# Performance work log

Hardware: AMD Instinct MI355X
Metric: run time of the kernel (lower is better)

## Reference

```python
import jax, jax.numpy as jnp
import numpy as np

N = 100001          # 1000 DAGs * (99 tasks + 1 summary) + 1 global node
E = 3200000
IN_DIM = 8
H = 64
N_DAGS = 1000
TEMPERATURE = 1.0


def setup_inputs() -> dict:
    key = jax.random.key(0)
    ks = jax.random.split(key, 12)
    x = jax.random.normal(ks[0], (N, IN_DIM), dtype=jnp.float32)
    flags = jax.random.bernoulli(ks[1], 0.5, (N,)).astype(jnp.float32)
    x = x.at[:, -1].set(flags)  # last feature column is the schedule flag
    edge_index = jax.random.randint(ks[2], (2, E), 0, N, dtype=jnp.int32)
    dag_summary_index = jnp.arange(N_DAGS, dtype=jnp.int32) * 100 + 99

    def w(k, shape, fan_in):
        return jax.random.normal(k, shape, dtype=jnp.float32) / np.float32(np.sqrt(fan_in))

    return {
        'x': x,
        'edge_index': edge_index,
        'dag_summary_index': dag_summary_index,
        'W1': w(ks[3], (IN_DIM, H), IN_DIM), 'b1': jnp.zeros((H,), jnp.float32),
        'W2': w(ks[4], (H, H), H),           'b2': jnp.zeros((H,), jnp.float32),
        'M1': w(ks[5], (3 * H, H), 3 * H),   'mb1': jnp.zeros((H,), jnp.float32),
        'M2': w(ks[6], (H, H), H),           'mb2': jnp.zeros((H,), jnp.float32),
        'M3': w(ks[7], (H, 1), H),           'mb3': jnp.zeros((1,), jnp.float32),
    }


def _gcn_conv(x, src, dst, W, b):
    # PyG GCNConv: add self-loops, symmetric normalization, linear, scatter-add, bias
    n = x.shape[0]
    loop = jnp.arange(n, dtype=src.dtype)
    s = jnp.concatenate([src, loop])
    d = jnp.concatenate([dst, loop])
    deg = jax.ops.segment_sum(jnp.ones_like(s, dtype=x.dtype), d, num_segments=n)
    dinv = jnp.where(deg > 0, jax.lax.rsqrt(deg), 0.0)
    norm = dinv[s] * dinv[d]                      # [E+N]
    h = x @ W                                     # [N, H]
    msg = h[s] * norm[:, None]                    # gather + scale (memory-bound)
    return jax.ops.segment_sum(msg, d, num_segments=n) + b


def reference(x, edge_index, dag_summary_index, W1, b1, W2, b2, M1, mb1, M2, mb2, M3, mb3):
    src, dst = edge_index[0], edge_index[1]
    h = jax.nn.relu(_gcn_conv(x, src, dst, W1, b1))
    h = jax.nn.relu(_gcn_conv(h, src, dst, W2, b2))   # [N, H]

    n = x.shape[0]
    idx = jnp.arange(n - 1)
    # dag_idx for node i == number of summary indices <= i (matches loop increment)
    dag_of = jnp.searchsorted(dag_summary_index, idx, side='right')
    dag_of = jnp.clip(dag_of, 0, dag_summary_index.shape[0] - 1)
    dag_emb = h[dag_summary_index[dag_of]]            # [N-1, H]
    global_emb = jnp.broadcast_to(h[-1], (n - 1, h.shape[1]))
    combined = jnp.concatenate([h[:-1], dag_emb, global_emb], axis=1)  # [N-1, 3H]

    z = jax.nn.relu(combined @ M1 + mb1)
    z = jax.nn.relu(z @ M2 + mb2)
    scores = (z @ M3 + mb3)[:, 0]                     # [N-1]

    flags = x[:-1, -1]
    is_summary = jnp.zeros((n,), bool).at[dag_summary_index].set(True)[:-1]
    mask = (flags == 1.0) & (~is_summary)
    probs = jax.nn.softmax(jnp.where(mask, scores / TEMPERATURE, -jnp.inf))
    selected = jnp.argmax(probs)                      # is_sampling=False path
    return probs, selected
```

## Files before the change

### kernel.cpp

```cpp
#include <hip/hip_runtime.h>
#include <math.h>

#define CHUNK 8192


__global__ void __launch_bounds__(256) k_bcount(const int* __restrict__ dst, int e,
                                                int* __restrict__ bcount) {
    __shared__ int c[256];
    int t = threadIdx.x;
    c[t] = 0;
    __syncthreads();
    for (int i = blockIdx.x * 256 + t; i < e; i += gridDim.x * 256)
        atomicAdd(&c[dst[i] >> 9], 1);
    __syncthreads();
    if (c[t]) atomicAdd(&bcount[t], c[t]);
}

__global__ void k_bscan(const int* __restrict__ bcount, int nb, int e,
                        int* __restrict__ bbase, int* __restrict__ bcur) {
    __shared__ int s[256];
    int t = threadIdx.x;
    int v = (t < nb) ? bcount[t] : 0;
    s[t] = v;
    __syncthreads();
    for (int d = 1; d < 256; d <<= 1) {
        int a = (t >= d) ? s[t - d] : 0;
        __syncthreads();
        s[t] += a;
        __syncthreads();
    }
    if (t < nb) { bbase[t] = s[t] - v; bcur[t] = s[t] - v; }
    if (t == 0) bbase[nb] = e;
}

__global__ void __launch_bounds__(256) k_bscatter(const int* __restrict__ src,
                                                  const int* __restrict__ dst, int e,
                                                  int* __restrict__ bcur,
                                                  int2* __restrict__ pairs) {
    __shared__ unsigned short rank[CHUNK];
    __shared__ int cnt[256];
    __shared__ int base[256];
    int t = threadIdx.x;
    int c0 = blockIdx.x * CHUNK;
    cnt[t] = 0;
    __syncthreads();
#pragma unroll
    for (int k = 0; k < CHUNK / 256; k++) {
        int i = c0 + k * 256 + t;
        if (i < e) {
            int b = dst[i] >> 9;
            rank[k * 256 + t] = (unsigned short)atomicAdd(&cnt[b], 1);
        }
    }
    __syncthreads();
    int cb = cnt[t];
    base[t] = cb ? atomicAdd(&bcur[t], cb) : 0;
    __syncthreads();
#pragma unroll
    for (int k = 0; k < CHUNK / 256; k++) {
        int i = c0 + k * 256 + t;
        if (i < e) {
            int d = dst[i];
            int b = d >> 9;
            pairs[base[b] + rank[k * 256 + t]] = make_int2(src[i], d);
        }
    }
}

__global__ void __launch_bounds__(256) k_bdeg(const int2* __restrict__ pairs,
                                              const int* __restrict__ bbase,
                                              int* __restrict__ deg, int* __restrict__ off,
                                              float* __restrict__ dinv, int n) {
    __shared__ int h[512];
    int t = threadIdx.x, b = blockIdx.x;
    h[t] = 0; h[t + 256] = 0;
    __syncthreads();
    int s0 = bbase[b], s1 = bbase[b + 1];
    int nbase = b << 9;
    for (int i = s0 + t; i < s1; i += 256)
        atomicAdd(&h[pairs[i].y - nbase], 1);
    __syncthreads();
    int o0 = h[t], o1 = h[t + 256];
    for (int d = 1; d < 512; d <<= 1) {
        int a0 = (t >= d) ? h[t - d] : 0;
        int a1 = (t + 256 >= d) ? h[t + 256 - d] : 0;
        __syncthreads();
        h[t] += a0; h[t + 256] += a1;
        __syncthreads();
    }
    int n0 = nbase + t, n1 = nbase + t + 256;
    if (n0 < n) { deg[n0] = o0; off[n0] = s0 + h[t] - o0; dinv[n0] = rsqrtf((float)(o0 + 1)); }
    if (n1 < n) { deg[n1] = o1; off[n1] = s0 + h[t + 256] - o1; dinv[n1] = rsqrtf((float)(o1 + 1)); }
}

__global__ void __launch_bounds__(256) k_bcsr(const int2* __restrict__ pairs,
                                              const int* __restrict__ bbase,
                                              const int* __restrict__ off,
                                              int* __restrict__ csr, int n) {
    __shared__ int curL[512];
    __shared__ int offL[512];
    int t = threadIdx.x, b = blockIdx.x;
    int nbase = b << 9;
    curL[t] = 0; curL[t + 256] = 0;
    int n0 = nbase + t, n1 = nbase + t + 256;
    offL[t] = (n0 < n) ? off[n0] : 0;
    offL[t + 256] = (n1 < n) ? off[n1] : 0;
    __syncthreads();
    int s0 = bbase[b], s1 = bbase[b + 1];
    for (int i = s0 + t; i < s1; i += 256) {
        int2 p = pairs[i];
        int local = p.y - nbase;
        int r = atomicAdd(&curL[local], 1);
        csr[offL[local] + r] = p.x;
    }
}


__global__ void k_xs(const float* __restrict__ x, const float* __restrict__ dinv,
                     float* __restrict__ xs, int n) {
    int t = blockIdx.x * blockDim.x + threadIdx.x;
    if (t >= n * 8) return;
    xs[t] = x[t] * dinv[t >> 3];
}


__global__ void __launch_bounds__(256) k_conv8(const float* __restrict__ xs,
                                               const int* __restrict__ csr,
                                               const int* __restrict__ off,
                                               const int* __restrict__ deg,
                                               float* __restrict__ agg1, int n) {
    int g = (blockIdx.x * 256 + threadIdx.x) >> 3;
    int lane = threadIdx.x & 7;
    if (g >= n) return;
    int base = off[g], cnt = deg[g];
    float acc = xs[g * 8 + lane];
    int e = 0;
    for (; e + 4 <= cnt; e += 4) {
        int s0 = csr[base + e];
        int s1 = csr[base + e + 1];
        int s2 = csr[base + e + 2];
        int s3 = csr[base + e + 3];
        acc += xs[s0 * 8 + lane];
        acc += xs[s1 * 8 + lane];
        acc += xs[s2 * 8 + lane];
        acc += xs[s3 * 8 + lane];
    }
    for (; e < cnt; e++) acc += xs[csr[base + e] * 8 + lane];
    agg1[g * 8 + lane] = acc;
}


__global__ void k_h1(const float* __restrict__ agg1, const float* __restrict__ W1,
                     const float* __restrict__ b1, const float* __restrict__ dinv,
                     float* __restrict__ H1s, int n) {
    int t = blockIdx.x * blockDim.x + threadIdx.x;
    int i = t >> 6, j = t & 63;
    if (i >= n) return;
    const float* ar = agg1 + (size_t)i * 8;
    float acc = 0.f;
#pragma unroll
    for (int k = 0; k < 8; k++) acc += ar[k] * W1[k * 64 + j];
    float dv = dinv[i];
    float h = fmaxf(dv * acc + b1[j], 0.f);
    H1s[(size_t)i * 64 + j] = h * dv;
}


__global__ void __launch_bounds__(256) k_conv64(const float* __restrict__ G,
                                                const int* __restrict__ csr,
                                                const int* __restrict__ off,
                                                const int* __restrict__ deg,
                                                float* __restrict__ agg2, int n) {
    int d = (blockIdx.x * 256 + threadIdx.x) >> 6;
    int j = threadIdx.x & 63;
    if (d >= n) return;
    int base = off[d], cnt = deg[d];
    float acc = G[(size_t)d * 64 + j];
    int e = 0;
    for (; e + 4 <= cnt; e += 4) {
        int s0 = csr[base + e];
        int s1 = csr[base + e + 1];
        int s2 = csr[base + e + 2];
        int s3 = csr[base + e + 3];
        acc += G[(size_t)s0 * 64 + j];
        acc += G[(size_t)s1 * 64 + j];
        acc += G[(size_t)s2 * 64 + j];
        acc += G[(size_t)s3 * 64 + j];
    }
    for (; e < cnt; e++) acc += G[(size_t)csr[base + e] * 64 + j];
    agg2[(size_t)d * 64 + j] = acc;
}


__global__ void __launch_bounds__(256) k_gw2b(const float* __restrict__ In,
                                              const float* __restrict__ W2,
                                              const float* __restrict__ b2,
                                              const float* __restrict__ dinv,
                                              float* __restrict__ Out, int n) {
    __shared__ float hs[128 * 65];
    __shared__ float ws[64 * 64];
    int tid = threadIdx.x;
    int base = blockIdx.x * 128;
#pragma unroll
    for (int m = 0; m < 4; m++) {
        int i = (m * 256 + tid) * 4;
        *(float4*)&ws[i] = *(const float4*)&W2[i];
    }
#pragma unroll
    for (int m = 0; m < 8; m++) {
        int idx = (m * 256 + tid) * 4;
        int node = idx >> 6, k = idx & 63;
        float4 v = *(const float4*)&In[(size_t)(base + node) * 64 + k];
        hs[node * 65 + k]     = v.x;
        hs[node * 65 + k + 1] = v.y;
        hs[node * 65 + k + 2] = v.z;
        hs[node * 65 + k + 3] = v.w;
    }
    __syncthreads();
    int jg = tid & 7, ng = tid >> 3;
    int j0 = jg * 8, n0 = ng * 4;
    float acc[4][8];
#pragma unroll
    for (int i = 0; i < 4; i++)
#pragma unroll
        for (int j = 0; j < 8; j++) acc[i][j] = 0.f;
#pragma unroll 4
    for (int k = 0; k < 64; k++) {
        float av[4];
#pragma unroll
        for (int i = 0; i < 4; i++) av[i] = hs[(n0 + i) * 65 + k];
        float bv[8];
        *(float4*)&bv[0] = *(float4*)&ws[k * 64 + j0];
        *(float4*)&bv[4] = *(float4*)&ws[k * 64 + j0 + 4];
#pragma unroll
        for (int i = 0; i < 4; i++)
#pragma unroll
            for (int j = 0; j < 8; j++) acc[i][j] += av[i] * bv[j];
    }
    float b2v[8];
    *(float4*)&b2v[0] = *(const float4*)&b2[j0];
    *(float4*)&b2v[4] = *(const float4*)&b2[j0 + 4];
#pragma unroll
    for (int i = 0; i < 4; i++) {
        int node = base + n0 + i;
        if (node < n) {
            float dv = dinv[node];
            float4 o0, o1;
            o0.x = fmaxf(acc[i][0] * dv + b2v[0], 0.f);
            o0.y = fmaxf(acc[i][1] * dv + b2v[1], 0.f);
            o0.z = fmaxf(acc[i][2] * dv + b2v[2], 0.f);
            o0.w = fmaxf(acc[i][3] * dv + b2v[3], 0.f);
            o1.x = fmaxf(acc[i][4] * dv + b2v[4], 0.f);
            o1.y = fmaxf(acc[i][5] * dv + b2v[5], 0.f);
            o1.z = fmaxf(acc[i][6] * dv + b2v[6], 0.f);
            o1.w = fmaxf(acc[i][7] * dv + b2v[7], 0.f);
            *(float4*)&Out[(size_t)node * 64 + j0]     = o0;
            *(float4*)&Out[(size_t)node * 64 + j0 + 4] = o1;
        }
    }
}


__global__ void k_dgt(const float* __restrict__ Hfin, const int* __restrict__ dsi,
                      const float* __restrict__ M1, const float* __restrict__ b1,
                      float* __restrict__ dgt, int n, int nd) {
    int w = (blockIdx.x * blockDim.x + threadIdx.x) >> 6;
    int lane = threadIdx.x & 63;
    if (w >= nd) return;
    float hd = Hfin[(size_t)dsi[w] * 64 + lane];
    float hg = Hfin[(size_t)(n - 1) * 64 + lane];
    float z = b1[lane];
#pragma unroll
    for (int k = 0; k < 64; k++) z += __shfl(hd, k) * M1[(64 + k) * 64 + lane];
#pragma unroll
    for (int k = 0; k < 64; k++) z += __shfl(hg, k) * M1[(128 + k) * 64 + lane];
    dgt[w * 64 + lane] = z;
}


__global__ void __launch_bounds__(256) k_mlp(const float* __restrict__ Hfin,
                                             const float* __restrict__ dgt,
                                             const float* __restrict__ x,
                                             const float* __restrict__ M1,
                                             const float* __restrict__ M2,
                                             const float* __restrict__ mb2,
                                             const float* __restrict__ M3,
                                             const float* __restrict__ mb3,
                                             float* __restrict__ scores, int n, int nd) {
    __shared__ float hs[128 * 65];
    __shared__ float ws[64 * 64];
    int tid = threadIdx.x;
    int base = blockIdx.x * 128;
#pragma unroll
    for (int m = 0; m < 4; m++) {
        int i = (m * 256 + tid) * 4;
        *(float4*)&ws[i] = *(const float4*)&M1[i];
    }
#pragma unroll
    for (int m = 0; m < 8; m++) {
        int idx = (m * 256 + tid) * 4;
        int node = idx >> 6, k = idx & 63;
        float4 v = *(const float4*)&Hfin[(size_t)(base + node) * 64 + k];
        hs[node * 65 + k]     = v.x;
        hs[node * 65 + k + 1] = v.y;
        hs[node * 65 + k + 2] = v.z;
        hs[node * 65 + k + 3] = v.w;
    }
    __syncthreads();
    int jg = tid & 7, ng = tid >> 3;
    int j0 = jg * 8, n0 = ng * 4;
    float acc[4][8];
#pragma unroll
    for (int i = 0; i < 4; i++)
#pragma unroll
        for (int j = 0; j < 8; j++) acc[i][j] = 0.f;
#pragma unroll 4
    for (int k = 0; k < 64; k++) {
        float av[4];
#pragma unroll
        for (int i = 0; i < 4; i++) av[i] = hs[(n0 + i) * 65 + k];
        float bv[8];
        *(float4*)&bv[0] = *(float4*)&ws[k * 64 + j0];
        *(float4*)&bv[4] = *(float4*)&ws[k * 64 + j0 + 4];
#pragma unroll
        for (int i = 0; i < 4; i++)
#pragma unroll
            for (int j = 0; j < 8; j++) acc[i][j] += av[i] * bv[j];
    }
    __syncthreads();
#pragma unroll
    for (int i = 0; i < 4; i++) {
        int node = base + n0 + i;
        int dago = (node + 1) / 100;
        if (dago >= nd) dago = nd - 1;
        float dv[8];
        *(float4*)&dv[0] = *(const float4*)&dgt[dago * 64 + j0];
        *(float4*)&dv[4] = *(const float4*)&dgt[dago * 64 + j0 + 4];
#pragma unroll
        for (int j = 0; j < 8; j++)
            hs[(n0 + i) * 65 + j0 + j] = fmaxf(acc[i][j] + dv[j], 0.f);
    }
#pragma unroll
    for (int m = 0; m < 4; m++) {
        int i = (m * 256 + tid) * 4;
        *(float4*)&ws[i] = *(const float4*)&M2[i];
    }
    __syncthreads();
    float acc2[4][8];
#pragma unroll
    for (int i = 0; i < 4; i++)
#pragma unroll
        for (int j = 0; j < 8; j++) acc2[i][j] = 0.f;
#pragma unroll 4
    for (int k = 0; k < 64; k++) {
        float av[4];
#pragma unroll
        for (int i = 0; i < 4; i++) av[i] = hs[(n0 + i) * 65 + k];
        float bv[8];
        *(float4*)&bv[0] = *(float4*)&ws[k * 64 + j0];
        *(float4*)&bv[4] = *(float4*)&ws[k * 64 + j0 + 4];
#pragma unroll
        for (int i = 0; i < 4; i++)
#pragma unroll
            for (int j = 0; j < 8; j++) acc2[i][j] += av[i] * bv[j];
    }
    float b2v[8], m3v[8];
    *(float4*)&b2v[0] = *(const float4*)&mb2[j0];
    *(float4*)&b2v[4] = *(const float4*)&mb2[j0 + 4];
    *(float4*)&m3v[0] = *(const float4*)&M3[j0];
    *(float4*)&m3v[4] = *(const float4*)&M3[j0 + 4];
    float b3 = mb3[0];
#pragma unroll
    for (int i = 0; i < 4; i++) {
        float p = 0.f;
#pragma unroll
        for (int j = 0; j < 8; j++) {
            float z2 = fmaxf(acc2[i][j] + b2v[j], 0.f);
            p += z2 * m3v[j];
        }
        p += __shfl_xor(p, 1);
        p += __shfl_xor(p, 2);
        p += __shfl_xor(p, 4);
        if (jg == 0) {
            int node = base + n0 + i;
            if (node < n - 1) {
                float flag = x[(size_t)node * 8 + 7];
                bool summary = ((node % 100) == 99);
                scores[node] = (flag == 1.0f && !summary) ? (p + b3) : -INFINITY;
            }
        }
    }
}


__global__ void k_red_max(const float* __restrict__ scores, int n,
                          float* __restrict__ pmax, int* __restrict__ pidx) {
    __shared__ float sv[256];
    __shared__ int si[256];
    float best = -INFINITY;
    int bi = 0x7fffffff;
    for (int i = blockIdx.x * 256 + threadIdx.x; i < n; i += gridDim.x * 256) {
        float v = scores[i];
        if (v > best || (v == best && i < bi)) { best = v; bi = i; }
    }
    sv[threadIdx.x] = best;
    si[threadIdx.x] = bi;
    __syncthreads();
    for (int o = 128; o; o >>= 1) {
        if (threadIdx.x < o) {
            float v = sv[threadIdx.x + o];
            int ix = si[threadIdx.x + o];
            if (v > sv[threadIdx.x] || (v == sv[threadIdx.x] && ix < si[threadIdx.x])) {
                sv[threadIdx.x] = v;
                si[threadIdx.x] = ix;
            }
        }
        __syncthreads();
    }
    if (threadIdx.x == 0) { pmax[blockIdx.x] = sv[0]; pidx[blockIdx.x] = si[0]; }
}

__global__ void k_red_max2(const float* __restrict__ pmax, const int* __restrict__ pidx,
                           int nb, float* __restrict__ finals, int* __restrict__ seli) {
    __shared__ float sv[256];
    __shared__ int si[256];
    int t = threadIdx.x;
    sv[t] = (t < nb) ? pmax[t] : -INFINITY;
    si[t] = (t < nb) ? pidx[t] : 0x7fffffff;
    __syncthreads();
    for (int o = 128; o; o >>= 1) {
        if (t < o) {
            float v = sv[t + o];
            int ix = si[t + o];
            if (v > sv[t] || (v == sv[t] && ix < si[t])) { sv[t] = v; si[t] = ix; }
        }
        __syncthreads();
    }
    if (t == 0) { finals[0] = sv[0]; seli[0] = si[0]; }
}

__global__ void k_red_sum(const float* __restrict__ scores, int n,
                          const float* __restrict__ finals, float* __restrict__ psum) {
    __shared__ float sv[256];
    float m = finals[0];
    float s = 0.f;
    for (int i = blockIdx.x * 256 + threadIdx.x; i < n; i += gridDim.x * 256)
        s += expf(scores[i] - m);
    sv[threadIdx.x] = s;
    __syncthreads();
    for (int o = 128; o; o >>= 1) {
        if (threadIdx.x < o) sv[threadIdx.x] += sv[threadIdx.x + o];
        __syncthreads();
    }
    if (threadIdx.x == 0) psum[blockIdx.x] = sv[0];
}

__global__ void k_red_sum2(const float* __restrict__ psum, int nb, float* __restrict__ finals) {
    __shared__ float sv[256];
    int t = threadIdx.x;
    sv[t] = (t < nb) ? psum[t] : 0.f;
    __syncthreads();
    for (int o = 128; o; o >>= 1) {
        if (t < o) sv[t] += sv[t + o];
        __syncthreads();
    }
    if (t == 0) finals[1] = sv[0];
}

__global__ void k_probs(const float* __restrict__ scores, const float* __restrict__ finals,
                        const int* __restrict__ seli, float* __restrict__ out, int n) {
    int i = blockIdx.x * 256 + threadIdx.x;
    float m = finals[0];
    float s = finals[1];
    if (i < n) out[i] = expf(scores[i] - m) / s;
    if (i == 0) out[n] = (float)seli[0];
}


extern "C" void kernel_launch(void* const* d_in, const int* in_sizes, int n_in,
                              void* d_out, int out_size, void* d_ws, size_t ws_size,
                              hipStream_t stream) {
    const float* x   = (const float*)d_in[0];
    const int*   ei  = (const int*)d_in[1];
    const int*   dsi = (const int*)d_in[2];
    const float* W1  = (const float*)d_in[3];
    const float* b1  = (const float*)d_in[4];
    const float* W2  = (const float*)d_in[5];
    const float* b2  = (const float*)d_in[6];
    const float* M1  = (const float*)d_in[7];
    const float* mb1 = (const float*)d_in[8];  (void)mb1;
    const float* M2  = (const float*)d_in[9];
    const float* mb2 = (const float*)d_in[10];
    const float* M3  = (const float*)d_in[11];
    const float* mb3 = (const float*)d_in[12];

    int N  = in_sizes[0] / 8;
    int E  = in_sizes[1] / 2;
    int ND = in_sizes[2];

    int N32 = (N + 63) & ~63;
    int NPAD = ((N + 127) / 128) * 128;
    int TILES = NPAD / 128;
    int nb = (N + 511) >> 9;

    char* p = (char*)d_ws;
    auto alloc = [&](size_t bytes) {
        char* r = p;
        p += (bytes + 255) & ~(size_t)255;
        return r;
    };
    int*   deg    = (int*)alloc((size_t)N32 * 4);
    int*   off    = (int*)alloc((size_t)N32 * 4);
    float* dinv   = (float*)alloc((size_t)N32 * 4);
    int*   csr    = (int*)alloc((size_t)E * 4);
    float* A      = (float*)alloc((size_t)NPAD * 64 * 4);
    float* B      = (float*)alloc((size_t)NPAD * 64 * 4);
    float* xs     = (float*)alloc((size_t)N32 * 8 * 4);
    float* agg1   = (float*)alloc((size_t)N32 * 8 * 4);
    float* dgt    = (float*)alloc((size_t)ND * 64 * 4);
    float* scores = (float*)alloc((size_t)N32 * 4);
    int*   bcount = (int*)alloc(256 * 4);
    int*   bbase  = (int*)alloc(257 * 4);
    int*   bcur   = (int*)alloc(256 * 4);
    float* pmax   = (float*)alloc(256 * 4);
    int*   pidx   = (int*)alloc(256 * 4);
    float* psum   = (float*)alloc(256 * 4);
    float* finals = (float*)alloc(16 * 4);
    int*   seli   = (int*)alloc(16 * 4);
    if ((size_t)(p - (char*)d_ws) > ws_size) return;

    int2* pairs = (int2*)A;

    const int* esrc = ei;
    const int* edst = ei + E;

    hipMemsetAsync(bcount, 0, 256 * 4, stream);
    k_bcount<<<512, 256, 0, stream>>>(edst, E, bcount);
    k_bscan<<<1, 256, 0, stream>>>(bcount, nb, E, bbase, bcur);
    k_bscatter<<<(E + CHUNK - 1) / CHUNK, 256, 0, stream>>>(esrc, edst, E, bcur, pairs);
    k_bdeg<<<nb, 256, 0, stream>>>(pairs, bbase, deg, off, dinv, N);
    k_bcsr<<<nb, 256, 0, stream>>>(pairs, bbase, off, csr, N);

    k_xs<<<(N * 8 + 255) / 256, 256, 0, stream>>>(x, dinv, xs, N);
    k_conv8<<<(N * 8 + 255) / 256, 256, 0, stream>>>(xs, csr, off, deg, agg1, N);
    k_h1<<<(N * 64 + 255) / 256, 256, 0, stream>>>(agg1, W1, b1, dinv, A, N);

    k_conv64<<<(N + 3) / 4, 256, 0, stream>>>(A, csr, off, deg, B, N);
    k_gw2b<<<TILES, 256, 0, stream>>>(B, W2, b2, dinv, B, N);

    k_dgt<<<(ND * 64 + 255) / 256, 256, 0, stream>>>(B, dsi, M1, b1, dgt, N, ND);
    k_mlp<<<TILES, 256, 0, stream>>>(B, dgt, x, M1, M2, mb2, M3, mb3, scores, N, ND);

    int NS = N - 1;
    k_red_max<<<256, 256, 0, stream>>>(scores, NS, pmax, pidx);
    k_red_max2<<<1, 256, 0, stream>>>(pmax, pidx, 256, finals, seli);
    k_red_sum<<<256, 256, 0, stream>>>(scores, NS, finals, psum);
    k_red_sum2<<<1, 256, 0, stream>>>(psum, 256, finals);
    k_probs<<<(NS + 256) / 256, 256, 0, stream>>>(scores, finals, seli, (float*)d_out, NS);
}
```

Baseline: 335.5 us.

## Pack edge pairs into 32-bit words, unroll conv64 gather, fuse softmax reductions

Edge pairs produced by the bucket scatter are packed into a single 32-bit word (source shifted left by 9, low 9 bits holding the local destination), which halves the traffic through the intermediate buffer. The conv64 gather now makes the node index wave-uniform with readfirstlane and issues eight neighbour loads before summing them, to keep more loads in flight. The separate max and sum-exp reductions are merged into one online-softmax pass plus a single combine kernel, removing two launches and one full read of the scores. Packing requires source indices below 2^23, which holds for this N, and the online softmax evaluates more expf calls per element.

```diff
diff --git a/kernel.cpp b/kernel.cpp
--- a/kernel.cpp
+++ b/kernel.cpp
@@ -36,7 +36,7 @@
 __global__ void __launch_bounds__(256) k_bscatter(const int* __restrict__ src,
                                                   const int* __restrict__ dst, int e,
                                                   int* __restrict__ bcur,
-                                                  int2* __restrict__ pairs) {
+                                                  unsigned* __restrict__ eu) {
     __shared__ unsigned short rank[CHUNK];
     __shared__ int cnt[256];
     __shared__ int base[256];
@@ -62,12 +62,13 @@
         if (i < e) {
             int d = dst[i];
             int b = d >> 9;
-            pairs[base[b] + rank[k * 256 + t]] = make_int2(src[i], d);
-        }
-    }
-}
-
-__global__ void __launch_bounds__(256) k_bdeg(const int2* __restrict__ pairs,
+            eu[base[b] + rank[k * 256 + t]] =
+                ((unsigned)src[i] << 9) | (unsigned)(d & 511);
+        }
+    }
+}
+
+__global__ void __launch_bounds__(256) k_bdeg(const unsigned* __restrict__ eu,
                                               const int* __restrict__ bbase,
                                               int* __restrict__ deg, int* __restrict__ off,
                                               float* __restrict__ dinv, int n) {
@@ -76,9 +77,8 @@
     h[t] = 0; h[t + 256] = 0;
     __syncthreads();
     int s0 = bbase[b], s1 = bbase[b + 1];
-    int nbase = b << 9;
     for (int i = s0 + t; i < s1; i += 256)
-        atomicAdd(&h[pairs[i].y - nbase], 1);
+        atomicAdd(&h[eu[i] & 511u], 1);
     __syncthreads();
     int o0 = h[t], o1 = h[t + 256];
     for (int d = 1; d < 512; d <<= 1) {
@@ -88,12 +88,13 @@
         h[t] += a0; h[t + 256] += a1;
         __syncthreads();
     }
+    int nbase = b << 9;
     int n0 = nbase + t, n1 = nbase + t + 256;
     if (n0 < n) { deg[n0] = o0; off[n0] = s0 + h[t] - o0; dinv[n0] = rsqrtf((float)(o0 + 1)); }
     if (n1 < n) { deg[n1] = o1; off[n1] = s0 + h[t + 256] - o1; dinv[n1] = rsqrtf((float)(o1 + 1)); }
 }
 
-__global__ void __launch_bounds__(256) k_bcsr(const int2* __restrict__ pairs,
+__global__ void __launch_bounds__(256) k_bcsr(const unsigned* __restrict__ eu,
                                               const int* __restrict__ bbase,
                                               const int* __restrict__ off,
                                               int* __restrict__ csr, int n) {
@@ -108,10 +109,10 @@
     __syncthreads();
     int s0 = bbase[b], s1 = bbase[b + 1];
     for (int i = s0 + t; i < s1; i += 256) {
-        int2 p = pairs[i];
-        int local = p.y - nbase;
+        unsigned p = eu[i];
+        int local = (int)(p & 511u);
         int r = atomicAdd(&curL[local], 1);
-        csr[offL[local] + r] = p.x;
+        csr[offL[local] + r] = (int)(p >> 9);
     }
 }
 
@@ -174,20 +175,22 @@
     int d = (blockIdx.x * 256 + threadIdx.x) >> 6;
     int j = threadIdx.x & 63;
     if (d >= n) return;
-    int base = off[d], cnt = deg[d];
-    float acc = G[(size_t)d * 64 + j];
+    int du = __builtin_amdgcn_readfirstlane(d);
+    int base = off[du], cnt = deg[du];
+    const float* Gj = G + j;
+    float acc = Gj[(size_t)du * 64];
     int e = 0;
-    for (; e + 4 <= cnt; e += 4) {
-        int s0 = csr[base + e];
-        int s1 = csr[base + e + 1];
-        int s2 = csr[base + e + 2];
-        int s3 = csr[base + e + 3];
-        acc += G[(size_t)s0 * 64 + j];
-        acc += G[(size_t)s1 * 64 + j];
-        acc += G[(size_t)s2 * 64 + j];
-        acc += G[(size_t)s3 * 64 + j];
-    }
-    for (; e < cnt; e++) acc += G[(size_t)csr[base + e] * 64 + j];
+    for (; e + 8 <= cnt; e += 8) {
+        int s[8];
+#pragma unroll
+        for (int u = 0; u < 8; u++) s[u] = csr[base + e + u];
+        float v[8];
+#pragma unroll
+        for (int u = 0; u < 8; u++) v[u] = Gj[(size_t)s[u] * 64];
+#pragma unroll
+        for (int u = 0; u < 8; u++) acc += v[u];
+    }
+    for (; e < cnt; e++) acc += Gj[(size_t)csr[base + e] * 64];
     agg2[(size_t)d * 64 + j] = acc;
 }
 
@@ -393,78 +396,71 @@
 }
 
 
-__global__ void k_red_max(const float* __restrict__ scores, int n,
-                          float* __restrict__ pmax, int* __restrict__ pidx) {
-    __shared__ float sv[256];
+__global__ void k_red_ms(const float* __restrict__ scores, int n,
+                         float* __restrict__ pm, float* __restrict__ ps,
+                         int* __restrict__ pidx) {
+    __shared__ float sm[256];
+    __shared__ float ss[256];
     __shared__ int si[256];
-    float best = -INFINITY;
+    float m = -INFINITY, s = 0.f;
     int bi = 0x7fffffff;
     for (int i = blockIdx.x * 256 + threadIdx.x; i < n; i += gridDim.x * 256) {
         float v = scores[i];
-        if (v > best || (v == best && i < bi)) { best = v; bi = i; }
-    }
-    sv[threadIdx.x] = best;
-    si[threadIdx.x] = bi;
+        if (v > m) {
+            s = s * expf(m - v) + 1.f;
+            m = v;
+            bi = i;
+        } else if (v != -INFINITY) {
+            s += expf(v - m);
+        }
+    }
+    sm[threadIdx.x] = m; ss[threadIdx.x] = s; si[threadIdx.x] = bi;
     __syncthreads();
     for (int o = 128; o; o >>= 1) {
         if (threadIdx.x < o) {
-            float v = sv[threadIdx.x + o];
-            int ix = si[threadIdx.x + o];
-            if (v > sv[threadIdx.x] || (v == sv[threadIdx.x] && ix < si[threadIdx.x])) {
-                sv[threadIdx.x] = v;
-                si[threadIdx.x] = ix;
-            }
+            float m2 = sm[threadIdx.x + o], s2 = ss[threadIdx.x + o];
+            int i2 = si[threadIdx.x + o];
+            float m1 = sm[threadIdx.x], s1 = ss[threadIdx.x];
+            int i1 = si[threadIdx.x];
+            float M = fmaxf(m1, m2);
+            float S = ((m1 == -INFINITY) ? 0.f : s1 * expf(m1 - M)) +
+                      ((m2 == -INFINITY) ? 0.f : s2 * expf(m2 - M));
+            int I;
+            if (m2 > m1 || (m2 == m1 && i2 < i1)) I = i2; else I = i1;
+            sm[threadIdx.x] = M; ss[threadIdx.x] = S; si[threadIdx.x] = I;
         }
         __syncthreads();
     }
-    if (threadIdx.x == 0) { pmax[blockIdx.x] = sv[0]; pidx[blockIdx.x] = si[0]; }
-}
-
-__global__ void k_red_max2(const float* __restrict__ pmax, const int* __restrict__ pidx,
-                           int nb, float* __restrict__ finals, int* __restrict__ seli) {
-    __shared__ float sv[256];
+    if (threadIdx.x == 0) { pm[blockIdx.x] = sm[0]; ps[blockIdx.x] = ss[0]; pidx[blockIdx.x] = si[0]; }
+}
+
+__global__ void k_red_comb(const float* __restrict__ pm, const float* __restrict__ ps,
+                           const int* __restrict__ pidx, int nb,
+                           float* __restrict__ finals, int* __restrict__ seli) {
+    __shared__ float sm[256];
+    __shared__ float ss[256];
     __shared__ int si[256];
     int t = threadIdx.x;
-    sv[t] = (t < nb) ? pmax[t] : -INFINITY;
+    sm[t] = (t < nb) ? pm[t] : -INFINITY;
+    ss[t] = (t < nb) ? ps[t] : 0.f;
     si[t] = (t < nb) ? pidx[t] : 0x7fffffff;
     __syncthreads();
     for (int o = 128; o; o >>= 1) {
         if (t < o) {
-            float v = sv[t + o];
-            int ix = si[t + o];
-            if (v > sv[t] || (v == sv[t] && ix < si[t])) { sv[t] = v; si[t] = ix; }
+            float m2 = sm[t + o], s2 = ss[t + o];
+            int i2 = si[t + o];
+            float m1 = sm[t], s1 = ss[t];
+            int i1 = si[t];
+            float M = fmaxf(m1, m2);
+            float S = ((m1 == -INFINITY) ? 0.f : s1 * expf(m1 - M)) +
+                      ((m2 == -INFINITY) ? 0.f : s2 * expf(m2 - M));
+            int I;
+            if (m2 > m1 || (m2 == m1 && i2 < i1)) I = i2; else I = i1;
+            sm[t] = M; ss[t] = S; si[t] = I;
         }
         __syncthreads();
     }
-    if (t == 0) { finals[0] = sv[0]; seli[0] = si[0]; }
-}
-
-__global__ void k_red_sum(const float* __restrict__ scores, int n,
-                          const float* __restrict__ finals, float* __restrict__ psum) {
-    __shared__ float sv[256];
-    float m = finals[0];
-    float s = 0.f;
-    for (int i = blockIdx.x * 256 + threadIdx.x; i < n; i += gridDim.x * 256)
-        s += expf(scores[i] - m);
-    sv[threadIdx.x] = s;
-    __syncthreads();
-    for (int o = 128; o; o >>= 1) {
-        if (threadIdx.x < o) sv[threadIdx.x] += sv[threadIdx.x + o];
-        __syncthreads();
-    }
-    if (threadIdx.x == 0) psum[blockIdx.x] = sv[0];
-}
-
-__global__ void k_red_sum2(const float* __restrict__ psum, int nb, float* __restrict__ finals) {
-    __shared__ float sv[256];
-    int t = threadIdx.x;
-    sv[t] = (t < nb) ? psum[t] : 0.f;
-    __syncthreads();
-    for (int o = 128; o; o >>= 1) {
-        if (t < o) sv[t] += sv[t + o];
-        __syncthreads();
-    }
-    if (t == 0) finals[1] = sv[0];
+    if (t == 0) { finals[0] = sm[0]; finals[1] = ss[0]; seli[0] = si[0]; }
 }
 
 __global__ void k_probs(const float* __restrict__ scores, const float* __restrict__ finals,
@@ -522,14 +518,14 @@
     int*   bcount = (int*)alloc(256 * 4);
     int*   bbase  = (int*)alloc(257 * 4);
     int*   bcur   = (int*)alloc(256 * 4);
-    float* pmax   = (float*)alloc(256 * 4);
+    float* pm     = (float*)alloc(256 * 4);
+    float* ps     = (float*)alloc(256 * 4);
     int*   pidx   = (int*)alloc(256 * 4);
-    float* psum   = (float*)alloc(256 * 4);
     float* finals = (float*)alloc(16 * 4);
     int*   seli   = (int*)alloc(16 * 4);
     if ((size_t)(p - (char*)d_ws) > ws_size) return;
 
-    int2* pairs = (int2*)A;
+    unsigned* eu = (unsigned*)A;
 
     const int* esrc = ei;
     const int* edst = ei + E;
@@ -537,9 +533,9 @@
     hipMemsetAsync(bcount, 0, 256 * 4, stream);
     k_bcount<<<512, 256, 0, stream>>>(edst, E, bcount);
     k_bscan<<<1, 256, 0, stream>>>(bcount, nb, E, bbase, bcur);
-    k_bscatter<<<(E + CHUNK - 1) / CHUNK, 256, 0, stream>>>(esrc, edst, E, bcur, pairs);
-    k_bdeg<<<nb, 256, 0, stream>>>(pairs, bbase, deg, off, dinv, N);
-    k_bcsr<<<nb, 256, 0, stream>>>(pairs, bbase, off, csr, N);
+    k_bscatter<<<(E + CHUNK - 1) / CHUNK, 256, 0, stream>>>(esrc, edst, E, bcur, eu);
+    k_bdeg<<<nb, 256, 0, stream>>>(eu, bbase, deg, off, dinv, N);
+    k_bcsr<<<nb, 256, 0, stream>>>(eu, bbase, off, csr, N);
 
     k_xs<<<(N * 8 + 255) / 256, 256, 0, stream>>>(x, dinv, xs, N);
     k_conv8<<<(N * 8 + 255) / 256, 256, 0, stream>>>(xs, csr, off, deg, agg1, N);
@@ -552,9 +548,7 @@
     k_mlp<<<TILES, 256, 0, stream>>>(B, dgt, x, M1, M2, mb2, M3, mb3, scores, N, ND);
 
     int NS = N - 1;
-    k_red_max<<<256, 256, 0, stream>>>(scores, NS, pmax, pidx);
-    k_red_max2<<<1, 256, 0, stream>>>(pmax, pidx, 256, finals, seli);
-    k_red_sum<<<256, 256, 0, stream>>>(scores, NS, finals, psum);
-    k_red_sum2<<<1, 256, 0, stream>>>(psum, 256, finals);
+    k_red_ms<<<256, 256, 0, stream>>>(scores, NS, pm, ps, pidx);
+    k_red_comb<<<1, 256, 0, stream>>>(pm, ps, pidx, 256, finals, seli);
     k_probs<<<(NS + 256) / 256, 256, 0, stream>>>(scores, finals, seli, (float*)d_out, NS);
 }
```

New measurement: 321.6 us. -4.1%, faster.
